# Kernel optimization log

Hardware: AMD Instinct MI355X
Metric: run time of the kernel (lower is better)

Reference implementation:

```python
import jax, jax.numpy as jnp
import numpy as np

B, V, FIN, K, FOUT, E = 8, 100000, 32, 4, 64, 800000


def setup_inputs() -> dict:
    key = jax.random.key(0)
    ks = jax.random.split(key, 6)
    inputs = jax.random.normal(ks[0], (B, V, FIN), dtype=jnp.float32)
    lap_rows = jax.random.randint(ks[1], (E,), 0, V, dtype=jnp.int32)
    lap_cols = jax.random.randint(ks[2], (E,), 0, V, dtype=jnp.int32)
    # rescaled-Laplacian nonzeros; small magnitude keeps the Chebyshev recurrence stable
    lap_vals = jax.random.normal(ks[3], (E,), dtype=jnp.float32) * 0.1
    # Kaiming-normal init: std = sqrt(2 / (Fin * K)) as in reset_parameters()
    std = float(np.sqrt(2.0 / (FIN * K)))
    weight = jax.random.normal(ks[4], (FIN, K, FOUT), dtype=jnp.float32) * std
    bias = jax.random.normal(ks[5], (FOUT,), dtype=jnp.float32) * 0.01
    return dict(inputs=inputs, lap_rows=lap_rows, lap_cols=lap_cols,
                lap_vals=lap_vals, weight=weight, bias=bias)


def reference(inputs, lap_rows, lap_cols, lap_vals, weight, bias):
    # inputs: [B, V, Fin]; weight: [Fin, K, Fout]; Laplacian in COO form.
    Bn, Vn, Fin = inputs.shape
    _, Kn, Fout = weight.shape

    def spmm(x):  # x: [V, Fin, B] -> L @ x via gather + segment-sum over edges
        msgs = lap_vals[:, None, None] * x[lap_cols]  # [E, Fin, B]
        return jax.ops.segment_sum(msgs, lap_rows, num_segments=Vn)

    x0 = jnp.transpose(inputs, (1, 2, 0))  # [V, Fin, B]
    xs = [x0]
    if Kn > 1:
        x1 = spmm(x0)
        xs.append(x1)
    for _ in range(2, Kn):
        x2 = 2.0 * spmm(x1) - x0  # Chebyshev recurrence T_k = 2 L T_{k-1} - T_{k-2}
        xs.append(x2)
        x0, x1 = x1, x2
    x = jnp.stack(xs, axis=0)  # [K, V, Fin, B]
    out = jnp.einsum('kvfb,fko->bvo', x, weight) + bias  # [B, V, Fout]
    return out
```

## Files before the change

kernel.cpp:

```cpp
#include <hip/hip_runtime.h>
#include <hip/hip_bf16.h>

#define B_    8
#define V_    100000
#define FIN_  32
#define K_    4
#define FOUT_ 64
#define E_    800000
#define NODE_F 256

typedef __attribute__((ext_vector_type(8))) short bf16x8;
typedef __attribute__((ext_vector_type(4))) float floatx4;

static __device__ inline float bf2f(unsigned short u) {
    unsigned int x = ((unsigned int)u) << 16;
    return __builtin_bit_cast(float, x);
}
static __device__ inline unsigned short f2bf(float f) {
    __hip_bfloat16 h = __float2bfloat16(f);
    return __builtin_bit_cast(unsigned short, h);
}

__global__ __launch_bounds__(256) void k_transpose(const float* __restrict__ in,
                                                   unsigned short* __restrict__ x0) {
    int tid = blockIdx.x * 256 + threadIdx.x;
    int f4 = tid & 7;
    int m  = tid >> 3;
    int v  = m >> 3;
    int b  = m & 7;
    float4 val = ((const float4*)(in + ((size_t)b * V_ + v) * FIN_))[f4];
    ushort4 o;
    o.x = f2bf(val.x); o.y = f2bf(val.y); o.z = f2bf(val.z); o.w = f2bf(val.w);
    ((ushort4*)x0)[tid] = o;
}

__global__ __launch_bounds__(256) void k_packw(const float* __restrict__ weight,
                                               unsigned short* __restrict__ wpack) {
    int t = blockIdx.x * 256 + threadIdx.x;
    int lane = t & 63;
    int ot   = (t >> 6) & 3;
    int kq   = t >> 8;
    int quad = lane >> 4, l16 = lane & 15;
    bf16x8 w;
    #pragma unroll
    for (int j = 0; j < 8; ++j)
        w[j] = (short)f2bf(weight[(size_t)(quad * 8 + j) * (K_ * FOUT_) + kq * FOUT_ + ot * 16 + l16]);
    *((bf16x8*)(wpack + (size_t)t * 8)) = w;
}

__global__ __launch_bounds__(256) void k_zero_int(int* __restrict__ p, int n) {
    int t = blockIdx.x * 256 + threadIdx.x;
    if (t < n) p[t] = 0;
}

__global__ __launch_bounds__(256) void k_hist(const int* __restrict__ rows,
                                              int* __restrict__ counts) {
    int e = blockIdx.x * 256 + threadIdx.x;
    if (e < E_) atomicAdd(&counts[rows[e]], 1);
}

__global__ __launch_bounds__(1024) void k_scan1(const int* __restrict__ counts,
                                                int* __restrict__ out,
                                                int* __restrict__ bsums, int n) {
    __shared__ int s[1024];
    int t = threadIdx.x;
    int idx = blockIdx.x * 1024 + t;
    int v = (idx < n) ? counts[idx] : 0;
    s[t] = v;
    __syncthreads();
    for (int off = 1; off < 1024; off <<= 1) {
        int add = (t >= off) ? s[t - off] : 0;
        __syncthreads();
        s[t] += add;
        __syncthreads();
    }
    if (idx < n) out[idx] = s[t] - v;
    if (t == 1023) bsums[blockIdx.x] = s[1023];
}

__global__ __launch_bounds__(128) void k_scan2(const int* __restrict__ bsums,
                                               int* __restrict__ boffs, int nb) {
    __shared__ int s[128];
    int t = threadIdx.x;
    int v = (t < nb) ? bsums[t] : 0;
    s[t] = v;
    __syncthreads();
    for (int off = 1; off < 128; off <<= 1) {
        int add = (t >= off) ? s[t - off] : 0;
        __syncthreads();
        s[t] += add;
        __syncthreads();
    }
    boffs[t] = s[t] - v;
}

__global__ __launch_bounds__(1024) void k_scan3(int* __restrict__ row_ptr,
                                                int* __restrict__ cursor,
                                                const int* __restrict__ boffs, int n) {
    int idx = blockIdx.x * 1024 + threadIdx.x;
    if (idx < n) {
        int r = row_ptr[idx] + boffs[blockIdx.x];
        row_ptr[idx] = r;
        cursor[idx]  = r;
    }
}

__global__ __launch_bounds__(256) void k_scatter(const int* __restrict__ rows,
                                                 const int* __restrict__ cols,
                                                 const float* __restrict__ vals,
                                                 int* __restrict__ cursor,
                                                 int2* __restrict__ e_pack) {
    int e = blockIdx.x * 256 + threadIdx.x;
    if (e < E_) {
        int r = rows[e];
        int pos = atomicAdd(&cursor[r], 1);
        e_pack[pos] = make_int2(cols[e], __float_as_int(vals[e]));
    }
}

__global__ __launch_bounds__(256) void k_spmm(const unsigned short* __restrict__ xc,
                                              const unsigned short* __restrict__ xp,
                                              const int* __restrict__ row_ptr,
                                              const int2* __restrict__ ep,
                                              unsigned short* __restrict__ xn,
                                              float scale, int has_prev) {
    int wave = threadIdx.x >> 6;
    int lane = threadIdx.x & 63;
    int half = lane >> 5;
    int hl   = lane & 31;
    int v = blockIdx.x * 4 + wave;
    if (v >= V_) return;
    int beg = row_ptr[v];
    int end = (v == V_ - 1) ? E_ : row_ptr[v + 1];

    float acc[8] = {0.f, 0.f, 0.f, 0.f, 0.f, 0.f, 0.f, 0.f};
    int e = beg + half;
    for (; e + 2 < end; e += 4) {
        int2 p0 = ep[e];
        int2 p1 = ep[e + 2];
        bf16x8 g0 = *((const bf16x8*)(xc + (size_t)p0.x * NODE_F + hl * 8));
        bf16x8 g1 = *((const bf16x8*)(xc + (size_t)p1.x * NODE_F + hl * 8));
        float v0 = __int_as_float(p0.y);
        float v1 = __int_as_float(p1.y);
        #pragma unroll
        for (int j = 0; j < 8; ++j) acc[j] += v0 * bf2f((unsigned short)g0[j]);
        #pragma unroll
        for (int j = 0; j < 8; ++j) acc[j] += v1 * bf2f((unsigned short)g1[j]);
    }
    for (; e < end; e += 2) {
        int2 p = ep[e];
        bf16x8 g = *((const bf16x8*)(xc + (size_t)p.x * NODE_F + hl * 8));
        float vv = __int_as_float(p.y);
        #pragma unroll
        for (int j = 0; j < 8; ++j) acc[j] += vv * bf2f((unsigned short)g[j]);
    }

    #pragma unroll
    for (int j = 0; j < 8; ++j) acc[j] += __shfl_xor(acc[j], 32);

    if (half == 0) {
        float r[8];
        if (has_prev) {
            bf16x8 p = *((const bf16x8*)(xp + (size_t)v * NODE_F + hl * 8));
            #pragma unroll
            for (int j = 0; j < 8; ++j) r[j] = scale * acc[j] - bf2f((unsigned short)p[j]);
        } else {
            #pragma unroll
            for (int j = 0; j < 8; ++j) r[j] = acc[j];
        }
        bf16x8 o;
        #pragma unroll
        for (int j = 0; j < 8; ++j) o[j] = (short)f2bf(r[j]);
        *((bf16x8*)(xn + (size_t)v * NODE_F + hl * 8)) = o;
    }
}

#define TILES_PER_WAVE 5
__global__ __launch_bounds__(256) void k_contract(const unsigned short* __restrict__ x0,
                                                  const unsigned short* __restrict__ x1,
                                                  const unsigned short* __restrict__ x2,
                                                  const unsigned short* __restrict__ x3,
                                                  const unsigned short* __restrict__ wpack,
                                                  const float* __restrict__ bias,
                                                  float* __restrict__ out) {
    int wave = threadIdx.x >> 6;
    int lane = threadIdx.x & 63;
    int quad = lane >> 4;
    int l16  = lane & 15;
    const unsigned short* xs[4] = {x0, x1, x2, x3};

    bf16x8 wfrag[4][4];
    #pragma unroll
    for (int kq = 0; kq < 4; ++kq)
        #pragma unroll
        for (int ot = 0; ot < 4; ++ot)
            wfrag[kq][ot] = *((const bf16x8*)(wpack + (size_t)((kq * 4 + ot) * 64 + lane) * 8));

    floatx4 bi[4];
    #pragma unroll
    for (int ot = 0; ot < 4; ++ot)
        bi[ot] = *((const floatx4*)(bias + ot * 16 + quad * 4));

    int wid   = blockIdx.x * 4 + wave;
    int tile0 = wid * TILES_PER_WAVE;
    #pragma unroll 1
    for (int t = 0; t < TILES_PER_WAVE; ++t) {
        int m0 = (tile0 + t) * 16;
        floatx4 acc[4] = {bi[0], bi[1], bi[2], bi[3]};
        #pragma unroll
        for (int kq = 0; kq < 4; ++kq) {
            bf16x8 xf = *((const bf16x8*)(xs[kq] + (size_t)(m0 + l16) * FIN_ + quad * 8));
            #pragma unroll
            for (int ot = 0; ot < 4; ++ot)
                acc[ot] = __builtin_amdgcn_mfma_f32_16x16x32_bf16(wfrag[kq][ot], xf, acc[ot], 0, 0, 0);
        }
        int m = m0 + l16;
        int v = m >> 3;
        int b = m & 7;
        float* op = out + ((size_t)b * V_ + v) * FOUT_ + quad * 4;
        #pragma unroll
        for (int ot = 0; ot < 4; ++ot)
            *((floatx4*)(op + ot * 16)) = acc[ot];
    }
}

extern "C" void kernel_launch(void* const* d_in, const int* in_sizes, int n_in,
                              void* d_out, int out_size, void* d_ws, size_t ws_size,
                              hipStream_t stream) {
    const float* inputs  = (const float*)d_in[0];
    const int*   laprows = (const int*)d_in[1];
    const int*   lapcols = (const int*)d_in[2];
    const float* lapvals = (const float*)d_in[3];
    const float* weight  = (const float*)d_in[4];
    const float* bias    = (const float*)d_in[5];
    float* out = (float*)d_out;

    const size_t XN = (size_t)V_ * NODE_F;
    unsigned short* x0 = (unsigned short*)d_ws;
    unsigned short* x1 = x0 + XN;
    unsigned short* x2 = x1 + XN;
    unsigned short* x3 = x2 + XN;
    int* counts  = (int*)(x3 + XN);
    int* row_ptr = counts + V_;
    int* cursor  = row_ptr + V_;
    int* bsums   = cursor + V_;
    int* boffs   = bsums + 128;
    int2* e_pack = (int2*)(boffs + 128);
    unsigned short* wpack = (unsigned short*)(e_pack + E_);

    const int NB_SCAN = (V_ + 1023) / 1024;

    hipLaunchKernelGGL(k_zero_int, dim3((V_ + 255) / 256), dim3(256), 0, stream, counts, V_);
    hipLaunchKernelGGL(k_packw, dim3(4), dim3(256), 0, stream, weight, wpack);
    hipLaunchKernelGGL(k_transpose, dim3((V_ * B_ * 8) / 256), dim3(256), 0, stream, inputs, x0);
    hipLaunchKernelGGL(k_hist, dim3((E_ + 255) / 256), dim3(256), 0, stream, laprows, counts);
    hipLaunchKernelGGL(k_scan1, dim3(NB_SCAN), dim3(1024), 0, stream, counts, row_ptr, bsums, V_);
    hipLaunchKernelGGL(k_scan2, dim3(1), dim3(128), 0, stream, bsums, boffs, NB_SCAN);
    hipLaunchKernelGGL(k_scan3, dim3(NB_SCAN), dim3(1024), 0, stream, row_ptr, cursor, boffs, V_);
    hipLaunchKernelGGL(k_scatter, dim3((E_ + 255) / 256), dim3(256), 0, stream,
                       laprows, lapcols, lapvals, cursor, e_pack);

    hipLaunchKernelGGL(k_spmm, dim3(V_ / 4), dim3(256), 0, stream,
                       x0, (const unsigned short*)nullptr, row_ptr, e_pack, x1, 1.0f, 0);
    hipLaunchKernelGGL(k_spmm, dim3(V_ / 4), dim3(256), 0, stream,
                       x1, x0, row_ptr, e_pack, x2, 2.0f, 1);
    hipLaunchKernelGGL(k_spmm, dim3(V_ / 4), dim3(256), 0, stream,
                       x2, x1, row_ptr, e_pack, x3, 2.0f, 1);

    hipLaunchKernelGGL(k_contract, dim3(2500), dim3(256), 0, stream,
                       x0, x1, x2, x3, wpack, bias, out);
}
```

Baseline: 631.0 us.

## Fuse setup kernels, defer scan offsets, and unroll SpMM gather by four

Folds the row histogram and weight packing into the transpose kernel, and drops the third scan pass. The per-1024-block offsets are now added where they are consumed, in scatter and SpMM. The SpMM edge loop gains a 4-edge-per-half-wave unrolled stage so more gathers are in flight. This removes several small launches and one pass over row_ptr, at the cost of an extra boffs load per row and higher register pressure in SpMM.

Result: no change. 626.5 us (-0.7%).

```diff
diff --git a/kernel.cpp b/kernel.cpp
--- a/kernel.cpp
+++ b/kernel.cpp
@@ -22,7 +22,11 @@
 }
 
 __global__ __launch_bounds__(256) void k_transpose(const float* __restrict__ in,
-                                                   unsigned short* __restrict__ x0) {
+                                                   unsigned short* __restrict__ x0,
+                                                   const int* __restrict__ rows,
+                                                   int* __restrict__ counts,
+                                                   const float* __restrict__ weight,
+                                                   unsigned short* __restrict__ wpack) {
     int tid = blockIdx.x * 256 + threadIdx.x;
     int f4 = tid & 7;
     int m  = tid >> 3;
@@ -32,20 +36,20 @@
     ushort4 o;
     o.x = f2bf(val.x); o.y = f2bf(val.y); o.z = f2bf(val.z); o.w = f2bf(val.w);
     ((ushort4*)x0)[tid] = o;
-}
-
-__global__ __launch_bounds__(256) void k_packw(const float* __restrict__ weight,
-                                               unsigned short* __restrict__ wpack) {
-    int t = blockIdx.x * 256 + threadIdx.x;
-    int lane = t & 63;
-    int ot   = (t >> 6) & 3;
-    int kq   = t >> 8;
-    int quad = lane >> 4, l16 = lane & 15;
-    bf16x8 w;
-    #pragma unroll
-    for (int j = 0; j < 8; ++j)
-        w[j] = (short)f2bf(weight[(size_t)(quad * 8 + j) * (K_ * FOUT_) + kq * FOUT_ + ot * 16 + l16]);
-    *((bf16x8*)(wpack + (size_t)t * 8)) = w;
+
+    if (tid < E_) atomicAdd(&counts[rows[tid]], 1);
+
+    if (tid < 1024) {
+        int lane = tid & 63;
+        int ot   = (tid >> 6) & 3;
+        int kq   = tid >> 8;
+        int quad = lane >> 4, l16 = lane & 15;
+        bf16x8 w;
+        #pragma unroll
+        for (int j = 0; j < 8; ++j)
+            w[j] = (short)f2bf(weight[(size_t)(quad * 8 + j) * (K_ * FOUT_) + kq * FOUT_ + ot * 16 + l16]);
+        *((bf16x8*)(wpack + (size_t)tid * 8)) = w;
+    }
 }
 
 __global__ __launch_bounds__(256) void k_zero_int(int* __restrict__ p, int n) {
@@ -53,14 +57,9 @@
     if (t < n) p[t] = 0;
 }
 
-__global__ __launch_bounds__(256) void k_hist(const int* __restrict__ rows,
-                                              int* __restrict__ counts) {
-    int e = blockIdx.x * 256 + threadIdx.x;
-    if (e < E_) atomicAdd(&counts[rows[e]], 1);
-}
-
 __global__ __launch_bounds__(1024) void k_scan1(const int* __restrict__ counts,
-                                                int* __restrict__ out,
+                                                int* __restrict__ row_ptr,
+                                                int* __restrict__ cursor,
                                                 int* __restrict__ bsums, int n) {
     __shared__ int s[1024];
     int t = threadIdx.x;
@@ -74,7 +73,11 @@
         s[t] += add;
         __syncthreads();
     }
-    if (idx < n) out[idx] = s[t] - v;
+    if (idx < n) {
+        int r = s[t] - v;
+        row_ptr[idx] = r;
+        cursor[idx]  = r;
+    }
     if (t == 1023) bsums[blockIdx.x] = s[1023];
 }
 
@@ -94,26 +97,16 @@
     boffs[t] = s[t] - v;
 }
 
-__global__ __launch_bounds__(1024) void k_scan3(int* __restrict__ row_ptr,
-                                                int* __restrict__ cursor,
-                                                const int* __restrict__ boffs, int n) {
-    int idx = blockIdx.x * 1024 + threadIdx.x;
-    if (idx < n) {
-        int r = row_ptr[idx] + boffs[blockIdx.x];
-        row_ptr[idx] = r;
-        cursor[idx]  = r;
-    }
-}
-
 __global__ __launch_bounds__(256) void k_scatter(const int* __restrict__ rows,
                                                  const int* __restrict__ cols,
                                                  const float* __restrict__ vals,
                                                  int* __restrict__ cursor,
+                                                 const int* __restrict__ boffs,
                                                  int2* __restrict__ e_pack) {
     int e = blockIdx.x * 256 + threadIdx.x;
     if (e < E_) {
         int r = rows[e];
-        int pos = atomicAdd(&cursor[r], 1);
+        int pos = atomicAdd(&cursor[r], 1) + boffs[r >> 10];
         e_pack[pos] = make_int2(cols[e], __float_as_int(vals[e]));
     }
 }
@@ -121,6 +114,7 @@
 __global__ __launch_bounds__(256) void k_spmm(const unsigned short* __restrict__ xc,
                                               const unsigned short* __restrict__ xp,
                                               const int* __restrict__ row_ptr,
+                                              const int* __restrict__ boffs,
                                               const int2* __restrict__ ep,
                                               unsigned short* __restrict__ xn,
                                               float scale, int has_prev) {
@@ -130,11 +124,33 @@
     int hl   = lane & 31;
     int v = blockIdx.x * 4 + wave;
     if (v >= V_) return;
-    int beg = row_ptr[v];
-    int end = (v == V_ - 1) ? E_ : row_ptr[v + 1];
+    int beg = row_ptr[v] + boffs[v >> 10];
+    int end = (v == V_ - 1) ? E_ : row_ptr[v + 1] + boffs[(v + 1) >> 10];
 
     float acc[8] = {0.f, 0.f, 0.f, 0.f, 0.f, 0.f, 0.f, 0.f};
     int e = beg + half;
+    for (; e + 6 < end; e += 8) {
+        int2 p0 = ep[e];
+        int2 p1 = ep[e + 2];
+        int2 p2 = ep[e + 4];
+        int2 p3 = ep[e + 6];
+        bf16x8 g0 = *((const bf16x8*)(xc + (size_t)p0.x * NODE_F + hl * 8));
+        bf16x8 g1 = *((const bf16x8*)(xc + (size_t)p1.x * NODE_F + hl * 8));
+        bf16x8 g2 = *((const bf16x8*)(xc + (size_t)p2.x * NODE_F + hl * 8));
+        bf16x8 g3 = *((const bf16x8*)(xc + (size_t)p3.x * NODE_F + hl * 8));
+        float v0 = __int_as_float(p0.y);
+        float v1 = __int_as_float(p1.y);
+        float v2 = __int_as_float(p2.y);
+        float v3 = __int_as_float(p3.y);
+        #pragma unroll
+        for (int j = 0; j < 8; ++j) acc[j] += v0 * bf2f((unsigned short)g0[j]);
+        #pragma unroll
+        for (int j = 0; j < 8; ++j) acc[j] += v1 * bf2f((unsigned short)g1[j]);
+        #pragma unroll
+        for (int j = 0; j < 8; ++j) acc[j] += v2 * bf2f((unsigned short)g2[j]);
+        #pragma unroll
+        for (int j = 0; j < 8; ++j) acc[j] += v3 * bf2f((unsigned short)g3[j]);
+    }
     for (; e + 2 < end; e += 4) {
         int2 p0 = ep[e];
         int2 p1 = ep[e + 2];
@@ -251,21 +267,20 @@
     const int NB_SCAN = (V_ + 1023) / 1024;
 
     hipLaunchKernelGGL(k_zero_int, dim3((V_ + 255) / 256), dim3(256), 0, stream, counts, V_);
-    hipLaunchKernelGGL(k_packw, dim3(4), dim3(256), 0, stream, weight, wpack);
-    hipLaunchKernelGGL(k_transpose, dim3((V_ * B_ * 8) / 256), dim3(256), 0, stream, inputs, x0);
-    hipLaunchKernelGGL(k_hist, dim3((E_ + 255) / 256), dim3(256), 0, stream, laprows, counts);
-    hipLaunchKernelGGL(k_scan1, dim3(NB_SCAN), dim3(1024), 0, stream, counts, row_ptr, bsums, V_);
+    hipLaunchKernelGGL(k_transpose, dim3((V_ * B_ * 8) / 256), dim3(256), 0, stream,
+                       inputs, x0, laprows, counts, weight, wpack);
+    hipLaunchKernelGGL(k_scan1, dim3(NB_SCAN), dim3(1024), 0, stream,
+                       counts, row_ptr, cursor, bsums, V_);
     hipLaunchKernelGGL(k_scan2, dim3(1), dim3(128), 0, stream, bsums, boffs, NB_SCAN);
-    hipLaunchKernelGGL(k_scan3, dim3(NB_SCAN), dim3(1024), 0, stream, row_ptr, cursor, boffs, V_);
     hipLaunchKernelGGL(k_scatter, dim3((E_ + 255) / 256), dim3(256), 0, stream,
-                       laprows, lapcols, lapvals, cursor, e_pack);
+                       laprows, lapcols, lapvals, cursor, boffs, e_pack);
 
     hipLaunchKernelGGL(k_spmm, dim3(V_ / 4), dim3(256), 0, stream,
-                       x0, (const unsigned short*)nullptr, row_ptr, e_pack, x1, 1.0f, 0);
+                       x0, (const unsigned short*)nullptr, row_ptr, boffs, e_pack, x1, 1.0f, 0);
     hipLaunchKernelGGL(k_spmm, dim3(V_ / 4), dim3(256), 0, stream,
-                       x1, x0, row_ptr, e_pack, x2, 2.0f, 1);
+                       x1, x0, row_ptr, boffs, e_pack, x2, 2.0f, 1);
     hipLaunchKernelGGL(k_spmm, dim3(V_ / 4), dim3(256), 0, stream,
-                       x2, x1, row_ptr, e_pack, x3, 2.0f, 1);
+                       x2, x1, row_ptr, boffs, e_pack, x3, 2.0f, 1);
 
     hipLaunchKernelGGL(k_contract, dim3(2500), dim3(256), 0, stream,
                        x0, x1, x2, x3, wpack, bias, out);
```
